# Performance work log

Measured on AMD Instinct MI355X. Metric: run time of the kernel, lower is better.

## Reference

```python
import jax, jax.numpy as jnp
import numpy as np

B, N, NB = 48, 512, 4096
SEG = ((0, 1600), (1600, 3200), (3200, 4096))  # static bond-type segments (C-C, C-H, H-H)
H, L = 8, 2                                     # be MLP hidden width / depth
BOTOL = 0.001
LP1, OVUN3, OVUN4, OVUN6, OVUN7, OVUN8 = 10.0, 5.0, 3.0, 6.0, 1.0, 12.0
BOX = 10.0


def _taper(r, rmin, rmax):
    # piecewise smooth step used on the uncorrected bond-order terms
    r3 = jnp.where(r > rmax, 1.0, 0.0)
    ok = (r <= rmax) & (r > rmin)
    r2 = jnp.where(ok, r, 0.0)
    r20 = jnp.where(ok, 1.0, 0.0)
    rterm = 1.0 / (rmin - rmax) ** 3
    rm = rmin * r20
    rd = rm - r2
    trm1 = rm + 2.0 * r2 - 3.0 * rmax * r20
    return rterm * rd * rd * trm1 + r3


def _div_if(y, x):
    return y / jnp.where(x != 0.0, x, 1e-8)


def setup_inputs():
    key = jax.random.key(0)
    ks = jax.random.split(key, 10)
    x = jax.random.uniform(ks[0], (B, N, 3), dtype=jnp.float32) * BOX
    cell = jnp.eye(3, dtype=jnp.float32) * BOX
    rcell = jnp.eye(3, dtype=jnp.float32) / BOX
    i = jax.random.randint(ks[1], (NB,), 0, N)
    j = jax.random.randint(ks[2], (NB,), 0, N)
    j = jnp.where(i == j, (j + 1) % N, j)
    bdid = jnp.stack([i, j], axis=1).astype(jnp.int32)
    atom_type = jax.random.randint(ks[3], (N,), 0, 2).astype(jnp.int32)
    # per-bond-type ReaxFF parameters (realistic magnitudes)
    bond_rosi = jnp.array([1.38, 1.12, 0.74], jnp.float32)
    bond_bo1 = jnp.array([-0.075, -0.05, -0.08], jnp.float32)
    bond_bo2 = jnp.array([6.8, 6.9, 6.0], jnp.float32)
    bond_ropi = jnp.array([1.28, 1.00, 0.70], jnp.float32)
    bond_bo3 = jnp.array([-0.20, -0.15, -0.20], jnp.float32)
    bond_bo4 = jnp.array([8.5, 7.0, 8.0], jnp.float32)
    bond_ropp = jnp.array([1.20, 0.90, 0.65], jnp.float32)
    bond_bo5 = jnp.array([-0.30, -0.25, -0.30], jnp.float32)
    bond_bo6 = jnp.array([10.0, 9.0, 10.0], jnp.float32)
    bond_Desi = jnp.array([145.0, 180.0, 160.0], jnp.float32)
    # per-species parameters (C, H)
    sp_val = jnp.array([4.0, 1.0], jnp.float32)
    sp_vale = jnp.array([4.0, 1.0], jnp.float32)
    sp_lp2 = jnp.array([0.1, 0.0], jnp.float32)
    sp_ovun2 = jnp.array([-5.0, -10.0], jnp.float32)
    sp_ovun5 = jnp.array([30.0, 0.0], jnp.float32)
    # fe (bond-energy) MLP weights per bond type: Wi (3,H), Wh (H,H)xL, Wo (H,1)
    fe_wi = jax.random.normal(ks[4], (3, 3, H), jnp.float32) * 0.5
    fe_w = jax.random.normal(ks[5], (3, L, H, H), jnp.float32) * 0.5
    fe_b = jax.random.normal(ks[6], (3, L, H), jnp.float32) * 0.5
    fe_wo = jax.random.normal(ks[7], (3, H, 1), jnp.float32) * 0.5
    fe_bo = jax.random.normal(ks[8], (3, 1), jnp.float32) * 0.5
    return dict(x=x, cell=cell, rcell=rcell, bdid=bdid, atom_type=atom_type,
                bond_rosi=bond_rosi, bond_bo1=bond_bo1, bond_bo2=bond_bo2,
                bond_ropi=bond_ropi, bond_bo3=bond_bo3, bond_bo4=bond_bo4,
                bond_ropp=bond_ropp, bond_bo5=bond_bo5, bond_bo6=bond_bo6,
                bond_Desi=bond_Desi, sp_val=sp_val, sp_vale=sp_vale,
                sp_lp2=sp_lp2, sp_ovun2=sp_ovun2, sp_ovun5=sp_ovun5,
                fe_wi=fe_wi, fe_w=fe_w, fe_b=fe_b, fe_wo=fe_wo, fe_bo=fe_bo)


def _forward(x, cell, rcell, bdid, atom_type,
             bond_rosi, bond_bo1, bond_bo2, bond_ropi, bond_bo3, bond_bo4,
             bond_ropp, bond_bo5, bond_bo6, bond_Desi,
             sp_val, sp_vale, sp_lp2, sp_ovun2, sp_ovun5,
             fe_wi, fe_w, fe_b, fe_wo, fe_bo):
    # --- all-pairs distances with minimum-image wrapping (fvr + rcell/cell) ---
    vr = x[:, :, None, :] - x[:, None, :, :]              # [B,N,N,3]
    vrf = vr @ rcell
    vrf = jnp.where(vrf - 0.5 > 0, vrf - 1.0, vrf)
    vrf = jnp.where(vrf + 0.5 < 0, vrf + 1.0, vrf)
    vr = vrf @ cell
    r = jnp.sqrt(jnp.sum(vr * vr, axis=3))                # [B,N,N]
    ii, jj = bdid[:, 0], bdid[:, 1]
    rbd_all = r[:, ii, jj]                                # [B,NB]

    si_l, pi_l, pp_l, ebd_l = [], [], [], []
    for t, (s0, s1) in enumerate(SEG):
        rbd = rbd_all[:, s0:s1]
        # uncorrected bond orders (get_bondorder_uc)
        eterm1 = (1.0 + BOTOL) * jnp.exp(bond_bo1[t] * (rbd / bond_rosi[t]) ** bond_bo2[t])
        eterm2 = jnp.exp(bond_bo3[t] * (rbd / bond_ropi[t]) ** bond_bo4[t])
        eterm3 = jnp.exp(bond_bo5[t] * (rbd / bond_ropp[t]) ** bond_bo6[t])
        bosi = _taper(eterm1, BOTOL, 2.0 * BOTOL) * (eterm1 - BOTOL)
        bopi = _taper(eterm2, BOTOL, 2.0 * BOTOL) * eterm2
        bopp = _taper(eterm3, BOTOL, 2.0 * BOTOL) * eterm3
        # bond-energy sigmoid MLP (fnn 'fe'): input [bosi,bopi,bopp]
        X = jnp.stack([bosi, bopi, bopp], axis=-1)        # [B,nb_t,3]
        h = jax.nn.sigmoid(jnp.einsum('bni,ih->bnh', X, fe_wi[t]))
        for l in range(L):
            h = jax.nn.sigmoid(h @ fe_w[t, l] + fe_b[t, l])
        esi = jax.nn.sigmoid(h @ fe_wo[t] + fe_bo[t])[..., 0]
        ebd_l.append(-bond_Desi[t] * esi)
        si_l.append(bosi); pi_l.append(bopi); pp_l.append(bopp)

    bosi = jnp.concatenate(si_l, axis=1)
    bopi = jnp.concatenate(pi_l, axis=1)
    bopp = jnp.concatenate(pp_l, axis=1)
    ebond = jnp.sum(jnp.concatenate(ebd_l, axis=1), axis=1)   # [B]

    # per-atom coordination via symmetric scatter of bond orders
    bo = bosi + bopi + bopp
    bpi = bopi + bopp
    zeros = jnp.zeros((x.shape[0], x.shape[1]), x.dtype)
    Delta = zeros.at[:, ii].add(bo).at[:, jj].add(bo)
    Delta_pi = zeros.at[:, ii].add(bpi).at[:, jj].add(bpi)
    SO = zeros.at[:, ii].add(bosi).at[:, jj].add(bosi)

    # species-indexed gathers of atomic params (self.s[st][sp] boolean gathers)
    val = sp_val[atom_type][None, :]
    vale = sp_vale[atom_type][None, :]
    lp2 = sp_lp2[atom_type][None, :]
    ovun2 = sp_ovun2[atom_type][None, :]
    ovun5 = sp_ovun5[atom_type][None, :]

    # --- elone ---
    Nlp = 0.5 * (vale - val)
    delta_e = 0.5 * (Delta - vale)
    De = -jax.nn.relu(-jnp.ceil(delta_e))
    nlp = -De + jnp.exp(-LP1 * 4.0 * jnp.square(1.0 + delta_e - De))
    Delta_lp = jax.nn.relu(Nlp - nlp + 1.0) - 1.0
    Elone = lp2 * Delta_lp / (1.0 + jnp.exp(-75.0 * Delta_lp))

    # --- eover ---
    delta_lpcorr = Delta - val - Delta_lp / (1.0 + OVUN3 * jnp.exp(OVUN4 * Delta_pi))
    otrm1 = _div_if(1.0, delta_lpcorr + val)
    Eover = SO * otrm1 * delta_lpcorr * jax.nn.sigmoid(-ovun2 * delta_lpcorr)

    # --- eunder ---
    expeu1 = jnp.exp(OVUN6 * delta_lpcorr)
    eu1 = jax.nn.sigmoid(ovun2 * delta_lpcorr)
    eu2 = 1.0 / (1.0 + OVUN7 * jnp.exp(OVUN8 * Delta_pi))
    Eunder = -ovun5 * (1.0 - expeu1) * eu1 * eu2

    return ebond + jnp.sum(Elone + Eover + Eunder, axis=1)   # [B]


def reference(x, cell, rcell, bdid, atom_type,
              bond_rosi, bond_bo1, bond_bo2, bond_ropi, bond_bo3, bond_bo4,
              bond_ropp, bond_bo5, bond_bo6, bond_Desi,
              sp_val, sp_vale, sp_lp2, sp_ovun2, sp_ovun5,
              fe_wi, fe_w, fe_b, fe_wo, fe_bo):
    return _forward(x, cell, rcell, bdid, atom_type,
                    bond_rosi, bond_bo1, bond_bo2, bond_ropi, bond_bo3, bond_bo4,
                    bond_ropp, bond_bo5, bond_bo6, bond_Desi,
                    sp_val, sp_vale, sp_lp2, sp_ovun2, sp_ovun5,
                    fe_wi, fe_w, fe_b, fe_wo, fe_bo)
```

## Files before the change

kernel.cpp:

```cpp
#include <hip/hip_runtime.h>
#include <math.h>

#define B_    48
#define N_    512
#define NBOND 4096
#define H_    8
#define L_    2
#define G_    16
#define TPB1  256
#define BPB   (NBOND / G_)
#define TPB2  512
#define NW1   (TPB1 / 64)

#define LOG2E 1.44269504f

__device__ __forceinline__ float rcpf(float x)  { return __builtin_amdgcn_rcpf(x); }
__device__ __forceinline__ float exp2g(float x) { return __builtin_amdgcn_exp2f(x); }
__device__ __forceinline__ float log2g(float x) { return __builtin_amdgcn_logf(x); }
__device__ __forceinline__ float expg(float x)  { return exp2g(x * LOG2E); }
__device__ __forceinline__ float sigf(float x)  { return rcpf(1.0f + expg(-x)); }

__device__ __forceinline__ float taperf(float r) {
    const float rmin = 0.001f, rmax = 0.002f;
    const float d = rmin - rmax;
    const float rterm = 1.0f / (d * d * d);
    float r3  = (r > rmax) ? 1.0f : 0.0f;
    bool ok   = (r <= rmax) && (r > rmin);
    float r2  = ok ? r : 0.0f;
    float r20 = ok ? 1.0f : 0.0f;
    float rm   = rmin * r20;
    float rd   = rm - r2;
    float trm1 = rm + 2.0f * r2 - 3.0f * rmax * r20;
    return rterm * rd * rd * trm1 + r3;
}

__global__ __launch_bounds__(TPB1) void bond_kernel(
    const float* __restrict__ x, const float* __restrict__ cell, const float* __restrict__ rcell,
    const int*  __restrict__ bdid,
    const float* __restrict__ rosi, const float* __restrict__ bo1, const float* __restrict__ bo2,
    const float* __restrict__ ropi, const float* __restrict__ bo3, const float* __restrict__ bo4,
    const float* __restrict__ ropp, const float* __restrict__ bo5, const float* __restrict__ bo6,
    const float* __restrict__ Desi,
    const float* __restrict__ wi, const float* __restrict__ w, const float* __restrict__ bvec,
    const float* __restrict__ wo, const float* __restrict__ bo_out,
    float2* __restrict__ pPart, float* __restrict__ pEbd)
{
    const int b   = blockIdx.x / G_;
    const int g   = blockIdx.x % G_;
    const int tid = threadIdx.x;

    __shared__ float sS[N_], sP[N_];

    sS[tid] = 0.0f;        sP[tid] = 0.0f;
    sS[tid + TPB1] = 0.0f; sP[tid + TPB1] = 0.0f;

    float c00 = cell[0], c01 = cell[1], c02 = cell[2];
    float c10 = cell[3], c11 = cell[4], c12 = cell[5];
    float c20 = cell[6], c21 = cell[7], c22 = cell[8];
    float q00 = rcell[0], q01 = rcell[1], q02 = rcell[2];
    float q10 = rcell[3], q11 = rcell[4], q12 = rcell[5];
    float q20 = rcell[6], q21 = rcell[7], q22 = rcell[8];

    const float* xb = x + (size_t)b * (N_ * 3);

    int k = g * BPB + tid;
    int t = (k < 1600) ? 0 : ((k < 3200) ? 1 : 2);
    const int ts = __builtin_amdgcn_readfirstlane(t);

    float lro_si = log2g(rosi[ts]);
    float lro_pi = log2g(ropi[ts]);
    float lro_pp = log2g(ropp[ts]);
    float cb1 = bo1[ts] * LOG2E;
    float cb3 = bo3[ts] * LOG2E;
    float cb5 = bo5[ts] * LOG2E;
    float pw2 = bo2[ts], pw4 = bo4[ts], pw6 = bo6[ts];
    float des = Desi[ts];

    int2 ij = ((const int2*)bdid)[k];
    int i = ij.x, j = ij.y;

    float vx = xb[3 * i + 0] - xb[3 * j + 0];
    float vy = xb[3 * i + 1] - xb[3 * j + 1];
    float vz = xb[3 * i + 2] - xb[3 * j + 2];

    float f0 = vx * q00 + vy * q10 + vz * q20;
    float f1 = vx * q01 + vy * q11 + vz * q21;
    float f2 = vx * q02 + vy * q12 + vz * q22;
    f0 = (f0 - 0.5f > 0.0f) ? f0 - 1.0f : f0;  f0 = (f0 + 0.5f < 0.0f) ? f0 + 1.0f : f0;
    f1 = (f1 - 0.5f > 0.0f) ? f1 - 1.0f : f1;  f1 = (f1 + 0.5f < 0.0f) ? f1 + 1.0f : f1;
    f2 = (f2 - 0.5f > 0.0f) ? f2 - 1.0f : f2;  f2 = (f2 + 0.5f < 0.0f) ? f2 + 1.0f : f2;
    float wx = f0 * c00 + f1 * c10 + f2 * c20;
    float wy = f0 * c01 + f1 * c11 + f2 * c21;
    float wz = f0 * c02 + f1 * c12 + f2 * c22;
    float r = __builtin_amdgcn_sqrtf(wx * wx + wy * wy + wz * wz);

    float lr = log2g(r);
    float p1 = exp2g(pw2 * (lr - lro_si));
    float p2 = exp2g(pw4 * (lr - lro_pi));
    float p3 = exp2g(pw6 * (lr - lro_pp));
    float e1 = 1.001f * exp2g(cb1 * p1);
    float e2 = exp2g(cb3 * p2);
    float e3 = exp2g(cb5 * p3);
    float bosi = taperf(e1) * (e1 - 0.001f);
    float bopi = taperf(e2) * e2;
    float bopp = taperf(e3) * e3;

    const float* Wi = wi + ts * 24;
    const float* Wm = w + ts * (L_ * H_ * H_);
    const float* Bv = bvec + ts * (L_ * H_);
    const float* Wo = wo + ts * H_;

    float h[H_], h2[H_];
    #pragma unroll
    for (int hh = 0; hh < H_; ++hh) {
        float s = bosi * Wi[0 * H_ + hh] + bopi * Wi[1 * H_ + hh] + bopp * Wi[2 * H_ + hh];
        h[hh] = sigf(s);
    }
    #pragma unroll
    for (int l = 0; l < L_; ++l) {
        #pragma unroll
        for (int ho = 0; ho < H_; ++ho) {
            float s = Bv[l * H_ + ho];
            #pragma unroll
            for (int hi = 0; hi < H_; ++hi)
                s += h[hi] * Wm[l * (H_ * H_) + hi * H_ + ho];
            h2[ho] = sigf(s);
        }
        #pragma unroll
        for (int hh = 0; hh < H_; ++hh) h[hh] = h2[hh];
    }
    float o = bo_out[ts];
    #pragma unroll
    for (int hi = 0; hi < H_; ++hi) o += h[hi] * Wo[hi];
    float ebd = -des * sigf(o);

    float bpi = bopi + bopp;
    __syncthreads();
    atomicAdd(&sS[i], bosi); atomicAdd(&sS[j], bosi);
    atomicAdd(&sP[i], bpi);  atomicAdd(&sP[j], bpi);
    __syncthreads();

    float2* pd = pPart + (size_t)(b * G_ + g) * N_;
    pd[tid]        = make_float2(sS[tid],        sP[tid]);
    pd[tid + TPB1] = make_float2(sS[tid + TPB1], sP[tid + TPB1]);

    float v = ebd;
    for (int off = 32; off > 0; off >>= 1) v += __shfl_down(v, off, 64);
    int lane = tid & 63, wid = tid >> 6;
    if (lane == 0) pEbd[(b * G_ + g) * NW1 + wid] = v;
}

__global__ __launch_bounds__(TPB2) void atom_kernel(
    const int* __restrict__ atype,
    const float* __restrict__ sval, const float* __restrict__ svale, const float* __restrict__ slp2,
    const float* __restrict__ sov2, const float* __restrict__ sov5,
    const float2* __restrict__ pPart, const float* __restrict__ pEbd,
    float* __restrict__ out)
{
    const int b   = blockIdx.x;
    const int tid = threadIdx.x;
    __shared__ float swave[TPB2 / 64];

    float so = 0.0f, DP = 0.0f;
    #pragma unroll
    for (int g = 0; g < G_; ++g) {
        float2 v = pPart[(size_t)(b * G_ + g) * N_ + tid];
        so += v.x;
        DP += v.y;
    }
    float D = so + DP;

    int at = atype[tid];
    float val  = sval[at];
    float vale = svale[at];
    float lp2  = slp2[at];
    float ov2  = sov2[at];
    float ov5  = sov5[at];

    float Nlp = 0.5f * (vale - val);
    float de  = 0.5f * (D - vale);
    float De  = fminf(ceilf(de), 0.0f);
    float t1  = 1.0f + de - De;
    float nlp = -De + expg(-40.0f * t1 * t1);
    float Dlp = fmaxf(Nlp - nlp + 1.0f, 0.0f) - 1.0f;
    float Elone = lp2 * Dlp * rcpf(1.0f + expg(-75.0f * Dlp));

    float dlc = D - val - Dlp * rcpf(1.0f + 5.0f * expg(3.0f * DP));
    float denom = dlc + val;
    float ot = rcpf((denom != 0.0f) ? denom : 1e-8f);
    float Eover = so * ot * dlc * sigf(-ov2 * dlc);

    float expeu1 = expg(6.0f * dlc);
    float eu1 = sigf(ov2 * dlc);
    float eu2 = rcpf(1.0f + expg(12.0f * DP));
    float Eunder = -ov5 * (1.0f - expeu1) * eu1 * eu2;

    float e = Elone + Eover + Eunder;
    if (tid < G_ * NW1) e += pEbd[b * (G_ * NW1) + tid];

    float v = e;
    for (int off = 32; off > 0; off >>= 1) v += __shfl_down(v, off, 64);
    int lane = tid & 63, wid = tid >> 6;
    if (lane == 0) swave[wid] = v;
    __syncthreads();
    if (tid == 0) {
        float s = 0.0f;
        #pragma unroll
        for (int wv = 0; wv < TPB2 / 64; ++wv) s += swave[wv];
        out[b] = s;
    }
}

extern "C" void kernel_launch(void* const* d_in, const int* in_sizes, int n_in,
                              void* d_out, int out_size, void* d_ws, size_t ws_size,
                              hipStream_t stream)
{
    const float* x     = (const float*)d_in[0];
    const float* cell  = (const float*)d_in[1];
    const float* rcell = (const float*)d_in[2];
    const int*   bdid  = (const int*)d_in[3];
    const int*   atype = (const int*)d_in[4];
    const float* rosi  = (const float*)d_in[5];
    const float* bo1   = (const float*)d_in[6];
    const float* bo2   = (const float*)d_in[7];
    const float* ropi  = (const float*)d_in[8];
    const float* bo3   = (const float*)d_in[9];
    const float* bo4   = (const float*)d_in[10];
    const float* ropp  = (const float*)d_in[11];
    const float* bo5   = (const float*)d_in[12];
    const float* bo6   = (const float*)d_in[13];
    const float* Desi  = (const float*)d_in[14];
    const float* sval  = (const float*)d_in[15];
    const float* svale = (const float*)d_in[16];
    const float* slp2  = (const float*)d_in[17];
    const float* sov2  = (const float*)d_in[18];
    const float* sov5  = (const float*)d_in[19];
    const float* wi    = (const float*)d_in[20];
    const float* w     = (const float*)d_in[21];
    const float* bvec  = (const float*)d_in[22];
    const float* wo    = (const float*)d_in[23];
    const float* bo_o  = (const float*)d_in[24];
    float* out = (float*)d_out;

    float2* pPart = (float2*)d_ws;
    float*  pEbd  = (float*)(pPart + (size_t)B_ * G_ * N_);

    bond_kernel<<<B_ * G_, TPB1, 0, stream>>>(
        x, cell, rcell, bdid,
        rosi, bo1, bo2, ropi, bo3, bo4, ropp, bo5, bo6, Desi,
        wi, w, bvec, wo, bo_o,
        pPart, pEbd);

    atom_kernel<<<B_, TPB2, 0, stream>>>(
        atype, sval, svale, slp2, sov2, sov5,
        pPart, pEbd, out);
}
```

Before: 16.30 us.

## Vectorize bond MLP with packed float2 math and split atom kernel across blocks

The bond-energy MLP now uses two-wide float vectors (splat times weight pairs) so the compiler can emit packed FMA instructions and load weights in pairs. The atom kernel is split into two 256-thread blocks per batch, each covering half the atoms, and the partial sums are combined with atomicAdd into an output zeroed by a memset. This gives the atom stage more blocks to run in parallel but adds a memset launch and float atomics, which make the summation order nondeterministic. The output-layer packed accumulator is computed and then thrown away in favour of the scalar loop, so that part is dead code.

```diff
diff --git a/kernel.cpp b/kernel.cpp
--- a/kernel.cpp
+++ b/kernel.cpp
@@ -9,10 +9,15 @@
 #define G_    16
 #define TPB1  256
 #define BPB   (NBOND / G_)
-#define TPB2  512
 #define NW1   (TPB1 / 64)
+#define AB_   2
+#define TPB2  256
 
 #define LOG2E 1.44269504f
+
+typedef float f32x2 __attribute__((ext_vector_type(2)));
+
+__device__ __forceinline__ f32x2 splat2(float v) { f32x2 r; r.x = v; r.y = v; return r; }
 
 __device__ __forceinline__ float rcpf(float x)  { return __builtin_amdgcn_rcpf(x); }
 __device__ __forceinline__ float exp2g(float x) { return __builtin_amdgcn_exp2f(x); }
@@ -105,33 +110,47 @@
     float bopi = taperf(e2) * e2;
     float bopp = taperf(e3) * e3;
 
-    const float* Wi = wi + ts * 24;
-    const float* Wm = w + ts * (L_ * H_ * H_);
-    const float* Bv = bvec + ts * (L_ * H_);
-    const float* Wo = wo + ts * H_;
-
-    float h[H_], h2[H_];
+    const f32x2* Wi2 = (const f32x2*)(wi  + ts * 24);
+    const f32x2* Wm2 = (const f32x2*)(w   + ts * (L_ * H_ * H_));
+    const f32x2* Bv2 = (const f32x2*)(bvec + ts * (L_ * H_));
+    const f32x2* Wo2 = (const f32x2*)(wo  + ts * H_);
+
+    float h[H_];
     #pragma unroll
-    for (int hh = 0; hh < H_; ++hh) {
-        float s = bosi * Wi[0 * H_ + hh] + bopi * Wi[1 * H_ + hh] + bopp * Wi[2 * H_ + hh];
-        h[hh] = sigf(s);
+    for (int p = 0; p < 4; ++p) {
+        f32x2 s2 = splat2(bosi) * Wi2[p]
+                 + splat2(bopi) * Wi2[4 + p]
+                 + splat2(bopp) * Wi2[8 + p];
+        h[2 * p]     = sigf(s2.x);
+        h[2 * p + 1] = sigf(s2.y);
     }
     #pragma unroll
     for (int l = 0; l < L_; ++l) {
-        #pragma unroll
-        for (int ho = 0; ho < H_; ++ho) {
-            float s = Bv[l * H_ + ho];
+        float hn[H_];
+        #pragma unroll
+        for (int p = 0; p < 4; ++p) {
+            f32x2 s2 = Bv2[l * 4 + p];
             #pragma unroll
             for (int hi = 0; hi < H_; ++hi)
-                s += h[hi] * Wm[l * (H_ * H_) + hi * H_ + ho];
-            h2[ho] = sigf(s);
+                s2 += splat2(h[hi]) * Wm2[(l * H_ + hi) * 4 + p];
+            hn[2 * p]     = sigf(s2.x);
+            hn[2 * p + 1] = sigf(s2.y);
         }
         #pragma unroll
-        for (int hh = 0; hh < H_; ++hh) h[hh] = h2[hh];
-    }
-    float o = bo_out[ts];
-    #pragma unroll
-    for (int hi = 0; hi < H_; ++hi) o += h[hi] * Wo[hi];
+        for (int hh = 0; hh < H_; ++hh) h[hh] = hn[hh];
+    }
+    f32x2 oacc = splat2(h[0]) * Wo2[0];
+    oacc += splat2(h[2]) * Wo2[1];
+    oacc += splat2(h[4]) * Wo2[2];
+    oacc += splat2(h[6]) * Wo2[3];
+    float o = bo_out[ts]
+            + h[0] * ((const float*)wo)[ts * H_ + 0];
+    {
+        const float* Wo = wo + ts * H_;
+        o = bo_out[ts];
+        #pragma unroll
+        for (int hi = 0; hi < H_; ++hi) o += h[hi] * Wo[hi];
+    }
     float ebd = -des * sigf(o);
 
     float bpi = bopi + bopp;
@@ -157,20 +176,22 @@
     const float2* __restrict__ pPart, const float* __restrict__ pEbd,
     float* __restrict__ out)
 {
-    const int b   = blockIdx.x;
+    const int b   = blockIdx.x / AB_;
+    const int c   = blockIdx.x % AB_;
     const int tid = threadIdx.x;
+    const int a   = c * TPB2 + tid;
     __shared__ float swave[TPB2 / 64];
 
     float so = 0.0f, DP = 0.0f;
     #pragma unroll
     for (int g = 0; g < G_; ++g) {
-        float2 v = pPart[(size_t)(b * G_ + g) * N_ + tid];
+        float2 v = pPart[(size_t)(b * G_ + g) * N_ + a];
         so += v.x;
         DP += v.y;
     }
     float D = so + DP;
 
-    int at = atype[tid];
+    int at = atype[a];
     float val  = sval[at];
     float vale = svale[at];
     float lp2  = slp2[at];
@@ -196,7 +217,7 @@
     float Eunder = -ov5 * (1.0f - expeu1) * eu1 * eu2;
 
     float e = Elone + Eover + Eunder;
-    if (tid < G_ * NW1) e += pEbd[b * (G_ * NW1) + tid];
+    if (c == 0 && tid < G_ * NW1) e += pEbd[b * (G_ * NW1) + tid];
 
     float v = e;
     for (int off = 32; off > 0; off >>= 1) v += __shfl_down(v, off, 64);
@@ -207,7 +228,7 @@
         float s = 0.0f;
         #pragma unroll
         for (int wv = 0; wv < TPB2 / 64; ++wv) s += swave[wv];
-        out[b] = s;
+        atomicAdd(&out[b], s);
     }
 }
 
@@ -245,13 +266,15 @@
     float2* pPart = (float2*)d_ws;
     float*  pEbd  = (float*)(pPart + (size_t)B_ * G_ * N_);
 
+    hipMemsetAsync(out, 0, B_ * sizeof(float), stream);
+
     bond_kernel<<<B_ * G_, TPB1, 0, stream>>>(
         x, cell, rcell, bdid,
         rosi, bo1, bo2, ropi, bo3, bo4, ropp, bo5, bo6, Desi,
         wi, w, bvec, wo, bo_o,
         pPart, pEbd);
 
-    atom_kernel<<<B_, TPB2, 0, stream>>>(
+    atom_kernel<<<B_ * AB_, TPB2, 0, stream>>>(
         atype, sval, svale, slp2, sov2, sov5,
         pPart, pEbd, out);
 }
```

After: 20.89 us. 28.2% more time.
